# Performance work log

Measured on AMD Instinct MI355X. Metric: run time of the kernel, lower is better.

The kernel has to match this reference:

```python
import jax, jax.numpy as jnp
import numpy as np

# TT ranks: source list [1,7,7,7,1] interpreted as r_0..r_4 with wraparound r_5 = r_0 = 1
RANKS = [1, 7, 7, 7, 1, 1]
LAYERS = [
    ([7, 4, 4, 4, 7], [8, 8, 8, 8, 4]),   # 3136 -> 16384
    ([8, 8, 8, 8, 4], [8, 8, 8, 4, 4]),   # 16384 -> 8192
    ([8, 8, 8, 4, 4], [8, 8, 4, 4, 4]),   # 8192 -> 4096
    ([8, 8, 4, 4, 4], [8, 4, 4, 4, 4]),   # 4096 -> 2048
    ([8, 4, 4, 4, 4], [10, 1, 1, 1, 1]),  # 2048 -> 10 (out_modes padded with 1s)
]
BATCH = 8192


def tt_linear(x, cores, bias):
    # x: [B, in_features]; cores[i]: [r_i, m_i, n_i, r_{i+1}]
    B = x.shape[0]
    t = x.reshape(B, -1, 1, 1)  # [B, M_remaining, N_done, r]
    for G in cores:
        r0, m, n, r1 = G.shape
        rest = t.shape[1] // m
        t = t.reshape(B, m, rest, t.shape[2], r0)
        # contract current input mode m and incoming rank r0 with the core
        t = jnp.einsum('bmsnp,pmoq->bsnoq', t, G)  # [B, rest, N_done, n, r1]
        t = t.reshape(B, rest, -1, r1)
    return t.reshape(B, -1) + bias  # [B, out_features]


def setup_inputs() -> dict:
    key = jax.random.key(0)
    keys = jax.random.split(key, 32)
    inp = {"x": jax.random.normal(keys[0], (BATCH, 3136), jnp.float32)}
    ki = 1
    for li, (im, om) in enumerate(LAYERS, start=1):
        for ci in range(5):
            shape = (RANKS[ci], im[ci], om[ci], RANKS[ci + 1])
            scale = 1.0 / np.sqrt(im[ci] * RANKS[ci])
            inp[f"l{li}_core{ci}"] = jax.random.normal(keys[ki], shape, jnp.float32) * scale
            ki += 1
        inp[f"l{li}_bias"] = jnp.zeros((int(np.prod(om)),), jnp.float32)
    return inp


def reference(x,
              l1_core0, l1_core1, l1_core2, l1_core3, l1_core4, l1_bias,
              l2_core0, l2_core1, l2_core2, l2_core3, l2_core4, l2_bias,
              l3_core0, l3_core1, l3_core2, l3_core3, l3_core4, l3_bias,
              l4_core0, l4_core1, l4_core2, l4_core3, l4_core4, l4_bias,
              l5_core0, l5_core1, l5_core2, l5_core3, l5_core4, l5_bias):
    h = jax.nn.relu(tt_linear(x, [l1_core0, l1_core1, l1_core2, l1_core3, l1_core4], l1_bias))
    h = jax.nn.relu(tt_linear(h, [l2_core0, l2_core1, l2_core2, l2_core3, l2_core4], l2_bias))
    h = jax.nn.relu(tt_linear(h, [l3_core0, l3_core1, l3_core2, l3_core3, l3_core4], l3_bias))
    h = jax.nn.relu(tt_linear(h, [l4_core0, l4_core1, l4_core2, l4_core3, l4_core4], l4_bias))
    logits = tt_linear(h, [l5_core0, l5_core1, l5_core2, l5_core3, l5_core4], l5_bias)
    return jax.nn.softmax(logits, axis=1)
```

## Files before the change

### kernel.cpp

```cpp
#include <hip/hip_runtime.h>
#include <stdint.h>
#include <stddef.h>

typedef _Float16 f16;
typedef _Float16 f16x8 __attribute__((ext_vector_type(8)));
typedef float    f32x4 __attribute__((ext_vector_type(4)));

#define NB 8192

struct Ptrs {
  const float *G0[5], *G1[5], *G2[5], *G3[5], *bias[5];
  float *T01[5], *T23[5], *biasr[5];
  f16   *WHt[5];
};

__global__ void prep1_kernel(Ptrs p) {
  constexpr int IM[5][5] = {{7,4,4,4,7},{8,8,8,8,4},{8,8,8,4,4},{8,8,4,4,4},{8,4,4,4,4}};
  constexpr int OM[5][5] = {{8,8,8,8,4},{8,8,8,4,4},{8,8,4,4,4},{8,4,4,4,4},{10,1,1,1,1}};
  const int job = blockIdx.x;
  const int tid = threadIdx.x;
  if (job < 5) {
    const int L = job;
    const int m1=IM[L][1], n0=OM[L][0], n1=OM[L][1];
    const int n01 = n0*n1;
    const int cnt = IM[L][0]*m1*n01*7;
    const float* G0 = p.G0[L]; const float* G1 = p.G1[L];
    float* T = p.T01[L];
    for (int e = tid; e < cnt; e += blockDim.x) {
      const int r2  = e % 7;
      const int j01 = (e/7) % n01;
      const int i01 = e / (7*n01);
      const int i0 = i01/m1, i1 = i01 - i0*m1;
      const int j0 = j01/n1, j1 = j01 - j0*n1;
      float s = 0.f;
      for (int r1 = 0; r1 < 7; ++r1)
        s += G0[(i0*n0 + j0)*7 + r1] * G1[((r1*m1 + i1)*n1 + j1)*7 + r2];
      T[e] = s;
    }
  } else if (job < 10) {
    const int L = job - 5;
    const int m2=IM[L][2], m3=IM[L][3], n2=OM[L][2], n3=OM[L][3];
    const int n23 = n2*n3;
    const int cnt = m2*m3*n23*7;
    const float* G2 = p.G2[L]; const float* G3 = p.G3[L];
    float* T = p.T23[L];
    for (int e = tid; e < cnt; e += blockDim.x) {
      const int r2  = e % 7;
      const int j23 = (e/7) % n23;
      const int i23 = e / (7*n23);
      const int i2 = i23/m3, i3 = i23 - i2*m3;
      const int j2 = j23/n3, j3 = j23 - j2*n3;
      float s = 0.f;
      for (int r3 = 0; r3 < 7; ++r3)
        s += G2[((r2*m2 + i2)*n2 + j2)*7 + r3] * G3[(r3*m3 + i3)*n3 + j3];
      T[e] = s;
    }
  } else {
    const int L = job - 10;
    constexpr int OUTF[5] = {16384, 8192, 4096, 2048, 10};
    constexpr int N4[5]   = {4,4,4,4,1};
    const int of = OUTF[L], n4 = N4[L], outH = of / n4;
    const float* b = p.bias[L];
    float* br = p.biasr[L];
    for (int e = tid; e < of; e += blockDim.x) {
      const int j4 = e / outH, jH = e - j4*outH;
      br[e] = b[jH*n4 + j4];
    }
  }
}

__global__ void prep2_kernel(Ptrs p) {
  constexpr int INH[5]  = {448, 4096, 2048, 1024, 512};
  constexpr int M23[5]  = {16, 64, 32, 16, 16};
  constexpr int N23[5]  = {64, 32, 16, 16, 1};
  constexpr int N01[5]  = {64, 64, 64, 32, 10};
  constexpr int BASE[6] = {0, 1835008, 10223616, 12320768, 12845056, 12850176};
  const int total = BASE[5];
  for (int e = blockIdx.x*blockDim.x + threadIdx.x; e < total;
       e += gridDim.x*blockDim.x) {
    int L = 0;
    while (L < 4 && e >= BASE[L+1]) ++L;
    const int le = e - BASE[L];
    const int iH = le % INH[L];
    const int jH = le / INH[L];
    const int i01 = iH / M23[L], i23 = iH - i01*M23[L];
    const int j01 = jH / N23[L], j23 = jH - j01*N23[L];
    const float* a = p.T01[L] + (i01*N01[L] + j01)*7;
    const float* b = p.T23[L] + (i23*N23[L] + j23)*7;
    float s = 0.f;
#pragma unroll
    for (int r = 0; r < 7; ++r) s += a[r]*b[r];
    p.WHt[L][le] = (f16)s;
  }
}

__global__ void stagea_x(const float* __restrict__ x, const float* __restrict__ g4,
                         f16* __restrict__ u, int BC) {
  const int idx = blockIdx.x*blockDim.x + threadIdx.x;
  if (idx >= BC*448) return;
  const int b = idx / 448, c = idx - b*448;
  const float* xr = x + (size_t)b*3136 + c*7;
  float v[7];
#pragma unroll
  for (int i = 0; i < 7; ++i) v[i] = xr[i];
#pragma unroll
  for (int j = 0; j < 4; ++j) {
    float s = 0.f;
#pragma unroll
    for (int i = 0; i < 7; ++i) s += v[i]*g4[i*4+j];
    u[(size_t)(b*4+j)*448 + c] = (f16)s;
  }
}

__global__ void __launch_bounds__(512, 2)
gemm256(const f16* __restrict__ A, const f16* __restrict__ Bt,
        f16* __restrict__ U, const float* __restrict__ biasr,
        const float* __restrict__ g4n,
        int N, int K, int n4n)
{
  __shared__ f16 Ls[2][2][256*64];

  const int tid  = threadIdx.x;
  const int wid  = tid >> 6, lane = tid & 63;
  const int wr   = wid >> 2, wc = wid & 3;
  const int l15  = lane & 15, l4 = lane >> 4, lm = l15 & 7;

  const int nwg = gridDim.x;
  int wg = blockIdx.x;
  if ((nwg & 7) == 0) wg = (wg & 7) * (nwg >> 3) + (wg >> 3);
  const int Nt = N >> 8;
  const int bx = wg / Nt, by = wg - bx * Nt;
  const int m0 = bx << 8, n0 = by << 8;

  const int rr   = tid >> 3;
  const int cs8  = (((tid & 7) ^ (rr & 7)) << 3);
  const int dst0 = tid << 3;

  int axoff[2], bxoff[2];
#pragma unroll
  for (int h = 0; h < 2; ++h) {
    const int cz = (((h << 2) + l4) ^ lm) << 3;
    axoff[h] = ((wr << 7) + l15) * 64 + cz;
    bxoff[h] = ((wc << 6) + l15) * 64 + cz;
  }

  f32x4 acc[8][4] = {};

  auto stage = [&](int buf, int kt) {
    const f16* gA = A + (size_t)m0 * K + kt;
    const f16* gB = Bt + (size_t)n0 * K + kt;
    f16* dA = &Ls[buf][0][0];
    f16* dB = &Ls[buf][1][0];
#pragma unroll
    for (int q = 0; q < 4; ++q)
      __builtin_amdgcn_global_load_lds(
          (const __attribute__((address_space(1))) void*)(gA + (size_t)(q*64 + rr)*K + cs8),
          (__attribute__((address_space(3))) void*)(dA + q*4096 + dst0), 16, 0, 0);
#pragma unroll
    for (int q = 0; q < 4; ++q)
      __builtin_amdgcn_global_load_lds(
          (const __attribute__((address_space(1))) void*)(gB + (size_t)(q*64 + rr)*K + cs8),
          (__attribute__((address_space(3))) void*)(dB + q*4096 + dst0), 16, 0, 0);
  };

  stage(0, 0);
  __syncthreads();
  const int nt = K >> 6;
  int cur = 0;
  for (int t = 0; t < nt; ++t) {
    if (t + 1 < nt) stage(cur ^ 1, (t + 1) << 6);
    __builtin_amdgcn_sched_barrier(0);
    const f16* As = &Ls[cur][0][0];
    const f16* Bs = &Ls[cur][1][0];
#pragma unroll
    for (int h = 0; h < 2; ++h) {
      f16x8 af[8], bf[4];
#pragma unroll
      for (int n = 0; n < 4; ++n) bf[n] = *(const f16x8*)(Bs + bxoff[h] + n*1024);
#pragma unroll
      for (int m = 0; m < 8; ++m) af[m] = *(const f16x8*)(As + axoff[h] + m*1024);
      __builtin_amdgcn_s_setprio(1);
#pragma unroll
      for (int m = 0; m < 8; ++m)
#pragma unroll
        for (int n = 0; n < 4; ++n)
          acc[m][n] = __builtin_amdgcn_mfma_f32_16x16x32_f16(af[m], bf[n], acc[m][n], 0, 0, 0);
      __builtin_amdgcn_s_setprio(0);
    }
    __syncthreads();
    cur ^= 1;
  }

#pragma unroll
  for (int m = 0; m < 8; ++m) {
    const int rb = m0 + (wr << 7) + (m << 4) + (l4 << 2);
    const int b  = rb >> 2;
#pragma unroll
    for (int n = 0; n < 4; ++n) {
      const int col = n0 + (wc << 6) + (n << 4) + l15;
      float v[4];
#pragma unroll
      for (int r = 0; r < 4; ++r)
        v[r] = fmaxf(acc[m][n][r] + biasr[(size_t)r * N + col], 0.f);
      if (n4n == 4) {
#pragma unroll
        for (int j = 0; j < 4; ++j) {
          float s = v[0]*g4n[j] + v[1]*g4n[4+j] + v[2]*g4n[8+j] + v[3]*g4n[12+j];
          U[(size_t)(b*4 + j) * N + col] = (f16)s;
        }
      } else {
        float s = v[0]*g4n[0] + v[1]*g4n[1] + v[2]*g4n[2] + v[3]*g4n[3];
        U[(size_t)b * N + col] = (f16)s;
      }
    }
  }
}

__global__ void __launch_bounds__(256, 2)
gemm_fused(const f16* __restrict__ A, const f16* __restrict__ Bt,
           f16* __restrict__ U, const float* __restrict__ biasr,
           const float* __restrict__ g4n,
           int N, int K, int n4n)
{
  __shared__ f16 Ls[2][2][128*64];

  const int tid  = threadIdx.x;
  const int wid  = tid >> 6, lane = tid & 63;
  const int wr   = wid >> 1, wc = wid & 1;
  const int l15  = lane & 15, l4 = lane >> 4, lm = l15 & 7;

  const int nwg = gridDim.x;
  int wg = blockIdx.x;
  if ((nwg & 7) == 0) wg = (wg & 7) * (nwg >> 3) + (wg >> 3);
  const int Nt = N >> 7;
  const int bx = wg / Nt, by = wg - bx * Nt;
  const int m0 = bx << 7, n0 = by << 7;

  const int rr   = tid >> 3;
  const int cs8  = (((tid & 7) ^ (rr & 7)) << 3);
  const int dst0 = wid << 9;

  int axoff[2], bxoff[2];
#pragma unroll
  for (int h = 0; h < 2; ++h) {
    const int cz = (((h << 2) + l4) ^ lm) << 3;
    axoff[h] = ((wr << 6) + l15) * 64 + cz;
    bxoff[h] = ((wc << 6) + l15) * 64 + cz;
  }

  f32x4 acc[4][4] = {};

  auto stage = [&](int buf, int kt) {
    const f16* gA = A + (size_t)m0 * K + kt;
    const f16* gB = Bt + (size_t)n0 * K + kt;
    f16* dA = &Ls[buf][0][0];
    f16* dB = &Ls[buf][1][0];
#pragma unroll
    for (int q = 0; q < 4; ++q)
      __builtin_amdgcn_global_load_lds(
          (const __attribute__((address_space(1))) void*)(gA + (size_t)(q*32 + rr)*K + cs8),
          (__attribute__((address_space(3))) void*)(dA + q*2048 + dst0), 16, 0, 0);
#pragma unroll
    for (int q = 0; q < 4; ++q)
      __builtin_amdgcn_global_load_lds(
          (const __attribute__((address_space(1))) void*)(gB + (size_t)(q*32 + rr)*K + cs8),
          (__attribute__((address_space(3))) void*)(dB + q*2048 + dst0), 16, 0, 0);
  };

  stage(0, 0);
  __syncthreads();
  const int nt = K >> 6;
  int cur = 0;
  for (int t = 0; t < nt; ++t) {
    if (t + 1 < nt) stage(cur ^ 1, (t + 1) << 6);
    __builtin_amdgcn_sched_barrier(0);
    const f16* As = &Ls[cur][0][0];
    const f16* Bs = &Ls[cur][1][0];
#pragma unroll
    for (int h = 0; h < 2; ++h) {
      f16x8 af[4], bf[4];
#pragma unroll
      for (int n = 0; n < 4; ++n) bf[n] = *(const f16x8*)(Bs + bxoff[h] + n*1024);
#pragma unroll
      for (int m = 0; m < 4; ++m) af[m] = *(const f16x8*)(As + axoff[h] + m*1024);
      __builtin_amdgcn_s_setprio(1);
#pragma unroll
      for (int m = 0; m < 4; ++m)
#pragma unroll
        for (int n = 0; n < 4; ++n)
          acc[m][n] = __builtin_amdgcn_mfma_f32_16x16x32_f16(af[m], bf[n], acc[m][n], 0, 0, 0);
      __builtin_amdgcn_s_setprio(0);
    }
    __syncthreads();
    cur ^= 1;
  }

#pragma unroll
  for (int m = 0; m < 4; ++m) {
    const int rb = m0 + (wr << 6) + (m << 4) + (l4 << 2);
    const int b  = rb >> 2;
#pragma unroll
    for (int n = 0; n < 4; ++n) {
      const int col = n0 + (wc << 6) + (n << 4) + l15;
      float v[4];
#pragma unroll
      for (int r = 0; r < 4; ++r)
        v[r] = fmaxf(acc[m][n][r] + biasr[(size_t)r * N + col], 0.f);
      if (n4n == 4) {
#pragma unroll
        for (int j = 0; j < 4; ++j) {
          float s = v[0]*g4n[j] + v[1]*g4n[4+j] + v[2]*g4n[8+j] + v[3]*g4n[12+j];
          U[(size_t)(b*4 + j) * N + col] = (f16)s;
        }
      } else {
        float s = v[0]*g4n[0] + v[1]*g4n[1] + v[2]*g4n[2] + v[3]*g4n[3];
        U[(size_t)b * N + col] = (f16)s;
      }
    }
  }
}

__global__ void l5_softmax(const f16* __restrict__ u, const f16* __restrict__ Wt,
                           const float* __restrict__ bias, float* __restrict__ out)
{
  const int wid = threadIdx.x >> 6, lane = threadIdx.x & 63;
  const int row = blockIdx.x*4 + wid;
  float acc[10] = {};
  const f16* ur = u + (size_t)row*512;
#pragma unroll
  for (int t = 0; t < 8; ++t) {
    const float a = (float)ur[t*64 + lane];
#pragma unroll
    for (int j = 0; j < 10; ++j)
      acc[j] += a * (float)Wt[j*512 + t*64 + lane];
  }
#pragma unroll
  for (int j = 0; j < 10; ++j) {
#pragma unroll
    for (int s = 32; s; s >>= 1) acc[j] += __shfl_xor(acc[j], s);
    acc[j] += bias[j];
  }
  float mx = acc[0];
#pragma unroll
  for (int j = 1; j < 10; ++j) mx = fmaxf(mx, acc[j]);
  float sum = 0.f;
#pragma unroll
  for (int j = 0; j < 10; ++j) { acc[j] = __expf(acc[j]-mx); sum += acc[j]; }
  const float inv = 1.f / sum;
  if (lane < 10) out[(size_t)row*10 + lane] = acc[lane]*inv;
}

extern "C" void kernel_launch(void* const* d_in, const int* in_sizes, int n_in,
                              void* d_out, int out_size, void* d_ws, size_t ws_size,
                              hipStream_t stream) {
  (void)in_sizes; (void)n_in; (void)out_size;
  const float* x = (const float*)d_in[0];
  Ptrs p;
  const float* G4[5];
  for (int L = 0; L < 5; ++L) {
    p.G0[L]   = (const float*)d_in[1 + L*6 + 0];
    p.G1[L]   = (const float*)d_in[1 + L*6 + 1];
    p.G2[L]   = (const float*)d_in[1 + L*6 + 2];
    p.G3[L]   = (const float*)d_in[1 + L*6 + 3];
    G4[L]     = (const float*)d_in[1 + L*6 + 4];
    p.bias[L] = (const float*)d_in[1 + L*6 + 5];
  }

  uintptr_t w = (uintptr_t)d_ws;
  auto alloc = [&](size_t bytes) {
    uintptr_t r = w; w += (bytes + 255) & ~(size_t)255; return (void*)r;
  };
  constexpr int  t01sz[5] = {12544, 28672, 28672, 14336, 2240};
  constexpr int  t23sz[5] = {7168, 14336, 3584, 1792, 112};
  constexpr int  brsz[5]  = {16384, 8192, 4096, 2048, 10};
  constexpr long whsz[5]  = {448L*4096, 4096L*2048, 2048L*1024, 1024L*512, 512L*10};
  for (int L = 0; L < 5; ++L) p.T01[L]   = (float*)alloc((size_t)t01sz[L]*4);
  for (int L = 0; L < 5; ++L) p.T23[L]   = (float*)alloc((size_t)t23sz[L]*4);
  for (int L = 0; L < 5; ++L) p.biasr[L] = (float*)alloc((size_t)brsz[L]*4);
  for (int L = 0; L < 5; ++L) p.WHt[L]   = (f16*)alloc((size_t)whsz[L]*2);
  const size_t fixedBytes = (size_t)(w - (uintptr_t)d_ws);

  int BC = 0;
  for (int c = NB; c >= 64; c >>= 1)
    if (fixedBytes + (size_t)c * (16384 + 32768) <= ws_size) { BC = c; break; }
  if (!BC) return;
  f16* bufA = (f16*)alloc((size_t)BC*16384);
  f16* bufB = (f16*)alloc((size_t)BC*32768);

  prep1_kernel<<<15, 256, 0, stream>>>(p);
  prep2_kernel<<<4096, 256, 0, stream>>>(p);

  const int nch = NB / BC;
  const int M   = BC * 4;
  for (int ch = 0; ch < nch; ++ch) {
    const size_t cs = (size_t)ch * BC;
    stagea_x<<<(BC*448 + 255)/256, 256, 0, stream>>>(x + cs*3136, G4[0], bufA, BC);
    gemm256<<<(M/256)*(4096/256), 512, 0, stream>>>(bufA, p.WHt[0], bufB, p.biasr[0],
                                                    G4[1], 4096, 448, 4);
    gemm256<<<(M/256)*(2048/256), 512, 0, stream>>>(bufB, p.WHt[1], bufA, p.biasr[1],
                                                    G4[2], 2048, 4096, 4);
    gemm256<<<(M/256)*(1024/256), 512, 0, stream>>>(bufA, p.WHt[2], bufB, p.biasr[2],
                                                    G4[3], 1024, 2048, 4);
    gemm_fused<<<(M/128)*(512/128), 256, 0, stream>>>(bufB, p.WHt[3], bufA, p.biasr[3],
                                                      G4[4], 512, 1024, 1);
    l5_softmax<<<BC/4, 256, 0, stream>>>(bufA, p.WHt[4], p.biasr[4],
                                         (float*)d_out + cs*10);
  }
}
```

Before: 970.1 us.

## Switch GEMM main loop to 4-stage K=32 LDS pipeline with explicit vmcnt waits

Replaces the double-buffered K=64 main loop of gemm256 with a four-buffer ring of K=32 tiles that is kept three tiles ahead. Each step waits with an explicit s_waitcnt on a fixed count of outstanding global-to-LDS loads instead of draining everything at a __syncthreads. The LDS layout and XOR swizzle change to match the new 32-wide tiles. The aim is to hide global load latency more deeply, at the cost of twice as many barriers per unit of K and a hand-tuned vmcnt count that must match the four loads issued per stage.

```diff
diff --git a/kernel.cpp b/kernel.cpp
--- a/kernel.cpp
+++ b/kernel.cpp
@@ -118,12 +118,12 @@
         const float* __restrict__ g4n,
         int N, int K, int n4n)
 {
-  __shared__ f16 Ls[2][2][256*64];
+  __shared__ f16 Ls[4][16384];
 
   const int tid  = threadIdx.x;
   const int wid  = tid >> 6, lane = tid & 63;
   const int wr   = wid >> 2, wc = wid & 3;
-  const int l15  = lane & 15, l4 = lane >> 4, lm = l15 & 7;
+  const int l15  = lane & 15, l4 = lane >> 4;
 
   const int nwg = gridDim.x;
   int wg = blockIdx.x;
@@ -132,64 +132,68 @@
   const int bx = wg / Nt, by = wg - bx * Nt;
   const int m0 = bx << 8, n0 = by << 8;
 
-  const int rr   = tid >> 3;
-  const int cs8  = (((tid & 7) ^ (rr & 7)) << 3);
+  const int sr0  = ((tid >> 3) << 1) | ((tid >> 2) & 1);
+  const int scol = (((tid & 3) ^ ((tid >> 3) & 3)) << 3);
   const int dst0 = tid << 3;
 
-  int axoff[2], bxoff[2];
-#pragma unroll
-  for (int h = 0; h < 2; ++h) {
-    const int cz = (((h << 2) + l4) ^ lm) << 3;
-    axoff[h] = ((wr << 7) + l15) * 64 + cz;
-    bxoff[h] = ((wc << 6) + l15) * 64 + cz;
-  }
+  const int laneF = (l15 >> 1)*64 + (l15 & 1)*32 + ((l4 ^ ((l15 >> 1) & 3)) << 3);
 
   f32x4 acc[8][4] = {};
-
-  auto stage = [&](int buf, int kt) {
+  const int nt = K >> 5;
+
+  auto stage = [&](int t) {
+    const int kt = t << 5;
+    f16* d = &Ls[t & 3][0];
     const f16* gA = A + (size_t)m0 * K + kt;
     const f16* gB = Bt + (size_t)n0 * K + kt;
-    f16* dA = &Ls[buf][0][0];
-    f16* dB = &Ls[buf][1][0];
-#pragma unroll
-    for (int q = 0; q < 4; ++q)
+#pragma unroll
+    for (int q = 0; q < 2; ++q)
       __builtin_amdgcn_global_load_lds(
-          (const __attribute__((address_space(1))) void*)(gA + (size_t)(q*64 + rr)*K + cs8),
-          (__attribute__((address_space(3))) void*)(dA + q*4096 + dst0), 16, 0, 0);
-#pragma unroll
-    for (int q = 0; q < 4; ++q)
+          (const __attribute__((address_space(1))) void*)(gA + (size_t)(q*128 + sr0)*K + scol),
+          (__attribute__((address_space(3))) void*)(d + q*4096 + dst0), 16, 0, 0);
+#pragma unroll
+    for (int q = 0; q < 2; ++q)
       __builtin_amdgcn_global_load_lds(
-          (const __attribute__((address_space(1))) void*)(gB + (size_t)(q*64 + rr)*K + cs8),
-          (__attribute__((address_space(3))) void*)(dB + q*4096 + dst0), 16, 0, 0);
+          (const __attribute__((address_space(1))) void*)(gB + (size_t)(q*128 + sr0)*K + scol),
+          (__attribute__((address_space(3))) void*)(d + 8192 + q*4096 + dst0), 16, 0, 0);
   };
 
-  stage(0, 0);
-  __syncthreads();
-  const int nt = K >> 6;
-  int cur = 0;
-  for (int t = 0; t < nt; ++t) {
-    if (t + 1 < nt) stage(cur ^ 1, (t + 1) << 6);
-    __builtin_amdgcn_sched_barrier(0);
-    const f16* As = &Ls[cur][0][0];
-    const f16* Bs = &Ls[cur][1][0];
-#pragma unroll
-    for (int h = 0; h < 2; ++h) {
-      f16x8 af[8], bf[4];
-#pragma unroll
-      for (int n = 0; n < 4; ++n) bf[n] = *(const f16x8*)(Bs + bxoff[h] + n*1024);
-#pragma unroll
-      for (int m = 0; m < 8; ++m) af[m] = *(const f16x8*)(As + axoff[h] + m*1024);
-      __builtin_amdgcn_s_setprio(1);
-#pragma unroll
-      for (int m = 0; m < 8; ++m)
-#pragma unroll
-        for (int n = 0; n < 4; ++n)
-          acc[m][n] = __builtin_amdgcn_mfma_f32_16x16x32_f16(af[m], bf[n], acc[m][n], 0, 0, 0);
-      __builtin_amdgcn_s_setprio(0);
-    }
-    __syncthreads();
-    cur ^= 1;
-  }
+  auto compute = [&](int b) {
+    const f16* As = &Ls[b][0];
+    const f16* Bs = &Ls[b][8192];
+    f16x8 af[8], bf[4];
+#pragma unroll
+    for (int n = 0; n < 4; ++n) bf[n] = *(const f16x8*)(Bs + wc*2048 + n*512 + laneF);
+#pragma unroll
+    for (int m = 0; m < 8; ++m) af[m] = *(const f16x8*)(As + wr*4096 + m*512 + laneF);
+    __builtin_amdgcn_s_setprio(1);
+#pragma unroll
+    for (int m = 0; m < 8; ++m)
+#pragma unroll
+      for (int n = 0; n < 4; ++n)
+        acc[m][n] = __builtin_amdgcn_mfma_f32_16x16x32_f16(af[m], bf[n], acc[m][n], 0, 0, 0);
+    __builtin_amdgcn_s_setprio(0);
+  };
+
+#define KTILE(T, VMS) do {                                        \
+    if ((T) + 3 < nt) stage((T) + 3);                             \
+    __builtin_amdgcn_sched_barrier(0);                            \
+    asm volatile("s_waitcnt vmcnt(" VMS ")" ::: "memory");        \
+    __builtin_amdgcn_sched_barrier(0);                            \
+    __builtin_amdgcn_s_barrier();                                 \
+    __builtin_amdgcn_sched_barrier(0);                            \
+    compute((T) & 3);                                             \
+    __builtin_amdgcn_sched_barrier(0);                            \
+    __builtin_amdgcn_s_barrier();                                 \
+    __builtin_amdgcn_sched_barrier(0);                            \
+  } while (0)
+
+  stage(0); stage(1); stage(2);
+  for (int t = 0; t < nt - 3; ++t) KTILE(t, "12");
+  KTILE(nt - 3, "8");
+  KTILE(nt - 2, "4");
+  KTILE(nt - 1, "0");
+#undef KTILE
 
 #pragma unroll
   for (int m = 0; m < 8; ++m) {
```

Measured after the change: 1.027 ms. +5.9%, slower.

## Software-pipeline LDS fragment loads against MFMAs with register double buffering

Applied to the files above, without the earlier changes.

Restructures the GEMM main loop so each k-tile's two half-steps use separate register fragment sets. LDS reads for the next half-step are issued before the current MFMA batch runs, and the second half's loads follow a lighter vmcnt plus s_barrier instead of __syncthreads. The aim is to hide LDS read latency behind MFMA execution. The cost is higher VGPR pressure from two live fragment sets and a peeled final iteration.

```diff
diff --git a/kernel.cpp b/kernel.cpp
--- a/kernel.cpp
+++ b/kernel.cpp
@@ -136,15 +136,15 @@
   const int cs8  = (((tid & 7) ^ (rr & 7)) << 3);
   const int dst0 = tid << 3;
 
-  int axoff[2], bxoff[2];
-#pragma unroll
-  for (int h = 0; h < 2; ++h) {
-    const int cz = (((h << 2) + l4) ^ lm) << 3;
-    axoff[h] = ((wr << 7) + l15) * 64 + cz;
-    bxoff[h] = ((wc << 6) + l15) * 64 + cz;
-  }
+  const int cz0 = ((l4 ^ lm)) << 3;
+  const int cz1 = ((4 + l4) ^ lm) << 3;
+  const int ax0 = ((wr << 7) + l15) * 64 + cz0;
+  const int ax1 = ((wr << 7) + l15) * 64 + cz1;
+  const int bx0 = ((wc << 6) + l15) * 64 + cz0;
+  const int bx1 = ((wc << 6) + l15) * 64 + cz1;
 
   f32x4 acc[8][4] = {};
+  f16x8 af0[8], bf0[4], af1[8], bf1[4];
 
   auto stage = [&](int buf, int kt) {
     const f16* gA = A + (size_t)m0 * K + kt;
@@ -164,31 +164,73 @@
   };
 
   stage(0, 0);
-  __syncthreads();
+  asm volatile("s_waitcnt vmcnt(0)" ::: "memory");
+  __builtin_amdgcn_s_barrier();
+#pragma unroll
+  for (int n = 0; n < 4; ++n) bf0[n] = *(const f16x8*)(&Ls[0][1][0] + bx0 + n*1024);
+#pragma unroll
+  for (int m = 0; m < 8; ++m) af0[m] = *(const f16x8*)(&Ls[0][0][0] + ax0 + m*1024);
+
   const int nt = K >> 6;
-  int cur = 0;
-  for (int t = 0; t < nt; ++t) {
-    if (t + 1 < nt) stage(cur ^ 1, (t + 1) << 6);
+  for (int t = 0; t < nt - 1; ++t) {
+    const int cur = t & 1;
+    stage(cur ^ 1, (t + 1) << 6);
     __builtin_amdgcn_sched_barrier(0);
+    {
+      const f16* As = &Ls[cur][0][0];
+      const f16* Bs = &Ls[cur][1][0];
+#pragma unroll
+      for (int n = 0; n < 4; ++n) bf1[n] = *(const f16x8*)(Bs + bx1 + n*1024);
+#pragma unroll
+      for (int m = 0; m < 8; ++m) af1[m] = *(const f16x8*)(As + ax1 + m*1024);
+    }
+    __builtin_amdgcn_s_setprio(1);
+#pragma unroll
+    for (int m = 0; m < 8; ++m)
+#pragma unroll
+      for (int n = 0; n < 4; ++n)
+        acc[m][n] = __builtin_amdgcn_mfma_f32_16x16x32_f16(af0[m], bf0[n], acc[m][n], 0, 0, 0);
+    __builtin_amdgcn_s_setprio(0);
+    __builtin_amdgcn_sched_barrier(0);
+    asm volatile("s_waitcnt vmcnt(0)" ::: "memory");
+    __builtin_amdgcn_s_barrier();
+    __builtin_amdgcn_sched_barrier(0);
+    {
+      const f16* As = &Ls[cur ^ 1][0][0];
+      const f16* Bs = &Ls[cur ^ 1][1][0];
+#pragma unroll
+      for (int n = 0; n < 4; ++n) bf0[n] = *(const f16x8*)(Bs + bx0 + n*1024);
+#pragma unroll
+      for (int m = 0; m < 8; ++m) af0[m] = *(const f16x8*)(As + ax0 + m*1024);
+    }
+    __builtin_amdgcn_s_setprio(1);
+#pragma unroll
+    for (int m = 0; m < 8; ++m)
+#pragma unroll
+      for (int n = 0; n < 4; ++n)
+        acc[m][n] = __builtin_amdgcn_mfma_f32_16x16x32_f16(af1[m], bf1[n], acc[m][n], 0, 0, 0);
+    __builtin_amdgcn_s_setprio(0);
+  }
+  {
+    const int cur = (nt - 1) & 1;
     const f16* As = &Ls[cur][0][0];
     const f16* Bs = &Ls[cur][1][0];
 #pragma unroll
-    for (int h = 0; h < 2; ++h) {
-      f16x8 af[8], bf[4];
-#pragma unroll
-      for (int n = 0; n < 4; ++n) bf[n] = *(const f16x8*)(Bs + bxoff[h] + n*1024);
-#pragma unroll
-      for (int m = 0; m < 8; ++m) af[m] = *(const f16x8*)(As + axoff[h] + m*1024);
-      __builtin_amdgcn_s_setprio(1);
-#pragma unroll
-      for (int m = 0; m < 8; ++m)
-#pragma unroll
-        for (int n = 0; n < 4; ++n)
-          acc[m][n] = __builtin_amdgcn_mfma_f32_16x16x32_f16(af[m], bf[n], acc[m][n], 0, 0, 0);
-      __builtin_amdgcn_s_setprio(0);
-    }
-    __syncthreads();
-    cur ^= 1;
+    for (int n = 0; n < 4; ++n) bf1[n] = *(const f16x8*)(Bs + bx1 + n*1024);
+#pragma unroll
+    for (int m = 0; m < 8; ++m) af1[m] = *(const f16x8*)(As + ax1 + m*1024);
+    __builtin_amdgcn_s_setprio(1);
+#pragma unroll
+    for (int m = 0; m < 8; ++m)
+#pragma unroll
+      for (int n = 0; n < 4; ++n)
+        acc[m][n] = __builtin_amdgcn_mfma_f32_16x16x32_f16(af0[m], bf0[n], acc[m][n], 0, 0, 0);
+#pragma unroll
+    for (int m = 0; m < 8; ++m)
+#pragma unroll
+      for (int n = 0; n < 4; ++n)
+        acc[m][n] = __builtin_amdgcn_mfma_f32_16x16x32_f16(af1[m], bf1[n], acc[m][n], 0, 0, 0);
+    __builtin_amdgcn_s_setprio(0);
   }
 
 #pragma unroll
```

New measurement: 953.3 us. Within noise of the previous version (-1.7%).

## Restructure GEMM main loop into four phases with interleaved half-tile prefetch

Applied to the files above, without the earlier changes.

Splits each 64-wide K step of the 256x256 MFMA GEMM into four output-quadrant phases. Each phase loads its A/B fragments from LDS, issues half of the next tile's global-to-LDS prefetch in the first two phases, and places explicit s_barrier and waitcnt fences around the MFMA block. The aim is to spread global loads and LDS reads across the compute so the memory and matrix pipes overlap with a ping-pong style schedule, replacing one bulk stage plus __syncthreads per iteration. The cost is more barriers per iteration and hand-placed waitcnt ordering, which could cause stalls or hazards if misordered.

```diff
diff --git a/kernel.cpp b/kernel.cpp
--- a/kernel.cpp
+++ b/kernel.cpp
@@ -136,59 +136,62 @@
   const int cs8  = (((tid & 7) ^ (rr & 7)) << 3);
   const int dst0 = tid << 3;
 
-  int axoff[2], bxoff[2];
-#pragma unroll
-  for (int h = 0; h < 2; ++h) {
-    const int cz = (((h << 2) + l4) ^ lm) << 3;
-    axoff[h] = ((wr << 7) + l15) * 64 + cz;
-    bxoff[h] = ((wc << 6) + l15) * 64 + cz;
-  }
-
   f32x4 acc[8][4] = {};
 
-  auto stage = [&](int buf, int kt) {
-    const f16* gA = A + (size_t)m0 * K + kt;
-    const f16* gB = Bt + (size_t)n0 * K + kt;
-    f16* dA = &Ls[buf][0][0];
-    f16* dB = &Ls[buf][1][0];
+  auto stage_half = [&](int buf, int kt, int h) {
+    const f16* g = (h ? Bt + (size_t)n0 * K : A + (size_t)m0 * K) + kt;
+    f16* d = &Ls[buf][h][0];
 #pragma unroll
     for (int q = 0; q < 4; ++q)
       __builtin_amdgcn_global_load_lds(
-          (const __attribute__((address_space(1))) void*)(gA + (size_t)(q*64 + rr)*K + cs8),
-          (__attribute__((address_space(3))) void*)(dA + q*4096 + dst0), 16, 0, 0);
-#pragma unroll
-    for (int q = 0; q < 4; ++q)
-      __builtin_amdgcn_global_load_lds(
-          (const __attribute__((address_space(1))) void*)(gB + (size_t)(q*64 + rr)*K + cs8),
-          (__attribute__((address_space(3))) void*)(dB + q*4096 + dst0), 16, 0, 0);
+          (const __attribute__((address_space(1))) void*)(g + (size_t)(q*64 + rr)*K + cs8),
+          (__attribute__((address_space(3))) void*)(d + q*4096 + dst0), 16, 0, 0);
   };
 
-  stage(0, 0);
-  __syncthreads();
+  stage_half(0, 0, 0); stage_half(0, 0, 1);
+  asm volatile("s_waitcnt vmcnt(0)" ::: "memory");
+  __builtin_amdgcn_s_barrier();
+
   const int nt = K >> 6;
-  int cur = 0;
   for (int t = 0; t < nt; ++t) {
-    if (t + 1 < nt) stage(cur ^ 1, (t + 1) << 6);
-    __builtin_amdgcn_sched_barrier(0);
+    const int cur = t & 1;
     const f16* As = &Ls[cur][0][0];
     const f16* Bs = &Ls[cur][1][0];
 #pragma unroll
-    for (int h = 0; h < 2; ++h) {
-      f16x8 af[8], bf[4];
-#pragma unroll
-      for (int n = 0; n < 4; ++n) bf[n] = *(const f16x8*)(Bs + bxoff[h] + n*1024);
-#pragma unroll
-      for (int m = 0; m < 8; ++m) af[m] = *(const f16x8*)(As + axoff[h] + m*1024);
+    for (int ph = 0; ph < 4; ++ph) {
+      const int mh = ph >> 1, nh = ph & 1;
+      f16x8 af[2][4], bf[2][2];
+#pragma unroll
+      for (int kh = 0; kh < 2; ++kh) {
+        const int cz = (((kh << 2) + l4) ^ lm) << 3;
+#pragma unroll
+        for (int m = 0; m < 4; ++m)
+          af[kh][m] = *(const f16x8*)(As + ((wr<<7) + (mh<<6) + (m<<4) + l15)*64 + cz);
+#pragma unroll
+        for (int n = 0; n < 2; ++n)
+          bf[kh][n] = *(const f16x8*)(Bs + ((wc<<6) + (nh<<5) + (n<<4) + l15)*64 + cz);
+      }
+      __builtin_amdgcn_sched_barrier(0);
+      if (t + 1 < nt && ph < 2) stage_half(cur ^ 1, (t + 1) << 6, ph);
+      __builtin_amdgcn_sched_barrier(0);
+      __builtin_amdgcn_s_barrier();
+      asm volatile("s_waitcnt lgkmcnt(0)" ::: "memory");
+      __builtin_amdgcn_sched_barrier(0);
       __builtin_amdgcn_s_setprio(1);
 #pragma unroll
-      for (int m = 0; m < 8; ++m)
-#pragma unroll
-        for (int n = 0; n < 4; ++n)
-          acc[m][n] = __builtin_amdgcn_mfma_f32_16x16x32_f16(af[m], bf[n], acc[m][n], 0, 0, 0);
+      for (int kh = 0; kh < 2; ++kh)
+#pragma unroll
+        for (int m = 0; m < 4; ++m)
+#pragma unroll
+          for (int n = 0; n < 2; ++n)
+            acc[(mh<<2)+m][(nh<<1)+n] = __builtin_amdgcn_mfma_f32_16x16x32_f16(
+                af[kh][m], bf[kh][n], acc[(mh<<2)+m][(nh<<1)+n], 0, 0, 0);
       __builtin_amdgcn_s_setprio(0);
-    }
-    __syncthreads();
-    cur ^= 1;
+      __builtin_amdgcn_sched_barrier(0);
+      if (ph == 3 && t + 1 < nt)
+        asm volatile("s_waitcnt vmcnt(0)" ::: "memory");
+      __builtin_amdgcn_s_barrier();
+    }
   }
 
 #pragma unroll
```

Measured after the change: 1.097 ms. 1.13x slower.
